# Performance work log

Measured on AMD Instinct MI355X. Metric: run time of the kernel, lower is better.

Reference implementation:

```python
import jax, jax.numpy as jnp
import numpy as np

N = 131072      # total nodes across batched molecular graphs
E = 524288      # directed edges (avg degree ~4)
G = 4096        # number of graphs in the batch
C_IN = 78       # atom feature dim
C_OUT = 128


def _init_linear(key, fan_in, fan_out):
    kw, kb = jax.random.split(key)
    s = 1.0 / np.sqrt(fan_in)
    W = jax.random.uniform(kw, (fan_in, fan_out), jnp.float32, -s, s)
    b = jax.random.uniform(kb, (fan_out,), jnp.float32, -s, s)
    return W, b


def setup_inputs() -> dict:
    key = jax.random.key(0)
    ks = jax.random.split(key, 8)
    x = jax.random.normal(ks[0], (N, C_IN), jnp.float32)
    edge_index = jax.random.randint(ks[1], (2, E), 0, N, dtype=jnp.int32)
    # sorted graph assignment, every graph non-empty (32 nodes per graph)
    batch = ((jnp.arange(N, dtype=jnp.int32) * G) // N).astype(jnp.int32)
    W1, b1 = _init_linear(ks[2], C_IN, C_IN)
    W2, b2 = _init_linear(ks[3], C_IN, 2 * C_IN)
    W3, b3 = _init_linear(ks[4], 2 * C_IN, 4 * C_IN)
    fcW, fcb = _init_linear(ks[5], 4 * C_IN, C_OUT)
    return {"x": x, "edge_index": edge_index, "batch": batch,
            "W1": W1, "b1": b1, "W2": W2, "b2": b2,
            "W3": W3, "b3": b3, "fcW": fcW, "fcb": fcb}


def _gcn_norm(edge_index, n):
    # PyG gcn_norm: add self-loops (weight 1), symmetric D^-1/2 A D^-1/2
    loop = jnp.arange(n, dtype=edge_index.dtype)
    src = jnp.concatenate([edge_index[0], loop])
    dst = jnp.concatenate([edge_index[1], loop])
    deg = jax.ops.segment_sum(jnp.ones_like(dst, jnp.float32), dst, num_segments=n)
    dis = jnp.where(deg > 0, jax.lax.rsqrt(jnp.maximum(deg, 1.0)), 0.0)
    norm = dis[src] * dis[dst]  # [E + N]
    return src, dst, norm


def _gcn_conv(h, W, b, src, dst, norm, n):
    h = h @ W                       # linear transform first (PyG order)
    msg = h[src] * norm[:, None]    # gather + edge-normalize
    agg = jax.ops.segment_sum(msg, dst, num_segments=n)  # scatter-add
    return agg + b


def reference(x, edge_index, batch, W1, b1, W2, b2, W3, b3, fcW, fcb):
    n = x.shape[0]
    src, dst, norm = _gcn_norm(edge_index, n)
    h = jax.nn.relu(_gcn_conv(x, W1, b1, src, dst, norm, n))
    h = jax.nn.relu(_gcn_conv(h, W2, b2, src, dst, norm, n))
    h = jax.nn.relu(_gcn_conv(h, W3, b3, src, dst, norm, n))
    pooled = jax.ops.segment_max(h, batch, num_segments=G)  # global max pool
    out = pooled @ fcW + fcb
    # dropout is identity in eval mode
    return out
```

## Files before the change

### kernel.cpp

```cpp
#include <hip/hip_runtime.h>

#define NN 131072
#define NE 524288
#define NG 4096

typedef __attribute__((ext_vector_type(8))) short bfx8;
typedef __attribute__((ext_vector_type(4))) float f32x4;

static __device__ __forceinline__ ushort f2bf(float f) {
    union { float f; unsigned u; } v; v.f = f;
    unsigned r = (v.u + 0x7fff + ((v.u >> 16) & 1)) >> 16;
    return (ushort)r;
}
static __device__ __forceinline__ float bf2f(short s) {
    union { unsigned u; float f; } v;
    v.u = ((unsigned)(ushort)s) << 16;
    return v.f;
}


__global__ void k_count(const int* __restrict__ dst, int* __restrict__ counts) {
    int e = blockIdx.x * blockDim.x + threadIdx.x;
    if (e < NE) atomicAdd(&counts[dst[e]], 1);
}

__global__ void k_scanA(const int* __restrict__ in, int* __restrict__ out,
                        int* __restrict__ bsum, float* __restrict__ dis) {
    __shared__ int s[256];
    int t = threadIdx.x;
    int i = blockIdx.x * 256 + t;
    int v = in[i];
    dis[i] = rsqrtf((float)(v + 1));
    s[t] = v;
    __syncthreads();
    for (int off = 1; off < 256; off <<= 1) {
        int x = (t >= off) ? s[t - off] : 0;
        __syncthreads();
        s[t] += x;
        __syncthreads();
    }
    out[i] = s[t] - v;
    if (t == 255) bsum[blockIdx.x] = s[t];
}

__global__ void k_scanB(int* __restrict__ bsum) {
    __shared__ int s[512];
    int t = threadIdx.x;
    int v = bsum[t];
    s[t] = v;
    __syncthreads();
    for (int off = 1; off < 512; off <<= 1) {
        int x = (t >= off) ? s[t - off] : 0;
        __syncthreads();
        s[t] += x;
        __syncthreads();
    }
    bsum[t] = s[t] - v;
}

__global__ void k_scanC(int* __restrict__ rowstart, const int* __restrict__ bsum) {
    int t = threadIdx.x;
    int i = blockIdx.x * 256 + t;
    rowstart[i] += bsum[blockIdx.x];
    if (i == 0) rowstart[NN] = NE;
}

__global__ void k_fill(const int* __restrict__ src, const int* __restrict__ dst,
                       const int* __restrict__ rowstart, int* __restrict__ cursor,
                       const float* __restrict__ dis,
                       int* __restrict__ col, float* __restrict__ wgt) {
    int e = blockIdx.x * blockDim.x + threadIdx.x;
    if (e >= NE) return;
    int s = src[e], d = dst[e];
    int pos = rowstart[d] + atomicAdd(&cursor[d], 1);
    col[pos] = s;
    wgt[pos] = dis[s] * dis[d];
}

__global__ void k_prep(const float* __restrict__ x, ushort* __restrict__ xb,
                       const float* __restrict__ W1, ushort* __restrict__ W1T,
                       const float* __restrict__ W2, ushort* __restrict__ W2T,
                       const float* __restrict__ W3, ushort* __restrict__ W3T) {
    int idx = blockIdx.x * 256 + threadIdx.x;
    const int NX = NN * 96;
    if (idx < NX) {
        int i = idx / 96, c = idx - i * 96;
        xb[idx] = (c < 78) ? f2bf(x[i * 78 + c]) : (ushort)0;
        return;
    }
    idx -= NX;
    if (idx < 78 * 96) {
        int n = idx / 96, k = idx - n * 96;
        W1T[idx] = (k < 78) ? f2bf(W1[k * 78 + n]) : (ushort)0;
        return;
    }
    idx -= 78 * 96;
    if (idx < 156 * 96) {
        int n = idx / 96, k = idx - n * 96;
        W2T[idx] = (k < 78) ? f2bf(W2[k * 156 + n]) : (ushort)0;
        return;
    }
    idx -= 156 * 96;
    if (idx < 312 * 160) {
        int n = idx / 160, k = idx - n * 160;
        W3T[idx] = (k < 156) ? f2bf(W3[k * 312 + n]) : (ushort)0;
    }
}


template<int KP, int LCH, int CO, int CPO, bool POOL>
__global__ __launch_bounds__(256)
void k_fused(const ushort* __restrict__ hin, const int* __restrict__ rowstart,
             const int* __restrict__ col, const float* __restrict__ wgt,
             const float* __restrict__ dis,
             const ushort* __restrict__ BT, const float* __restrict__ bias,
             const int* __restrict__ batch,
             ushort* __restrict__ hout, float* __restrict__ pooled) {
    constexpr int NCH = KP / 8;
    constexpr int LP  = LCH * 8;
    constexpr int NP  = (CO + 63) / 64;
    __shared__ ushort sA[64 * LP];

    const int tid  = threadIdx.x;
    const int row0 = blockIdx.x * 64;

    for (int id = tid; id < 64 * NCH; id += 256) {
        int r  = id / NCH, kc = id - r * NCH;
        int i  = row0 + r;
        int ch = kc * 8;
        const ushort* gb = hin + ch;

        float d = dis[i];
        bfx8 self = *(const bfx8*)(hin + (size_t)i * KP + ch);
        float acc[8];
        #pragma unroll
        for (int k = 0; k < 8; ++k) acc[k] = d * d * bf2f(self[k]);

        int j = rowstart[i], j1 = rowstart[i + 1];
        for (; j + 4 <= j1; j += 4) {
            int c0 = col[j], c1 = col[j + 1], c2 = col[j + 2], c3 = col[j + 3];
            float w0 = wgt[j], w1 = wgt[j + 1], w2 = wgt[j + 2], w3 = wgt[j + 3];
            bfx8 g0 = *(const bfx8*)(gb + (size_t)c0 * KP);
            bfx8 g1 = *(const bfx8*)(gb + (size_t)c1 * KP);
            bfx8 g2 = *(const bfx8*)(gb + (size_t)c2 * KP);
            bfx8 g3 = *(const bfx8*)(gb + (size_t)c3 * KP);
            #pragma unroll
            for (int k = 0; k < 8; ++k) {
                acc[k] = fmaf(w0, bf2f(g0[k]), acc[k]);
                acc[k] = fmaf(w1, bf2f(g1[k]), acc[k]);
                acc[k] = fmaf(w2, bf2f(g2[k]), acc[k]);
                acc[k] = fmaf(w3, bf2f(g3[k]), acc[k]);
            }
        }
        for (; j < j1; ++j) {
            int c = col[j];
            float w = wgt[j];
            bfx8 g = *(const bfx8*)(gb + (size_t)c * KP);
            #pragma unroll
            for (int k = 0; k < 8; ++k) acc[k] = fmaf(w, bf2f(g[k]), acc[k]);
        }

        bfx8 ov;
        #pragma unroll
        for (int k = 0; k < 8; ++k) ov[k] = (short)f2bf(acc[k]);
        int swz = (kc & ~7) | ((kc & 7) ^ (r & 7));
        *(bfx8*)(sA + r * LP + swz * 8) = ov;
    }
    __syncthreads();

    const int lane = tid & 63;
    const int wave = tid >> 6;
    const int wr = wave >> 1, wc = wave & 1;
    const int l15 = lane & 15, l4 = lane >> 4;
    const int r7 = l15 & 7;
    const int rowA0 = wr * 32 + l15;
    const int gbase = row0 + wr * 32;
    const int koff = l4 * 8;

    #pragma unroll
    for (int p = 0; p < NP; ++p) {
        const int bc0 = p * 64 + wc * 32 + l15;
        f32x4 acc[2][2] = {};
        #pragma unroll
        for (int ks = 0; ks < KP / 32; ++ks) {
            int chunk = l4 + ks * 4;
            int swz = (chunk & ~7) | ((chunk & 7) ^ r7);
            int off = swz * 8;
            bfx8 a0 = *(const bfx8*)(sA + rowA0 * LP + off);
            bfx8 a1 = *(const bfx8*)(sA + (rowA0 + 16) * LP + off);
            bfx8 b0 = {0,0,0,0,0,0,0,0}, b1 = {0,0,0,0,0,0,0,0};
            if (bc0 < CO)      b0 = *(const bfx8*)(BT + (size_t)bc0 * KP + koff + ks * 32);
            if (bc0 + 16 < CO) b1 = *(const bfx8*)(BT + (size_t)(bc0 + 16) * KP + koff + ks * 32);
            acc[0][0] = __builtin_amdgcn_mfma_f32_16x16x32_bf16(a0, b0, acc[0][0], 0, 0, 0);
            acc[0][1] = __builtin_amdgcn_mfma_f32_16x16x32_bf16(a0, b1, acc[0][1], 0, 0, 0);
            acc[1][0] = __builtin_amdgcn_mfma_f32_16x16x32_bf16(a1, b0, acc[1][0], 0, 0, 0);
            acc[1][1] = __builtin_amdgcn_mfma_f32_16x16x32_bf16(a1, b1, acc[1][1], 0, 0, 0);
        }

        if constexpr (POOL) {
            const bool uni = (batch[gbase] == batch[gbase + 31]);
            #pragma unroll
            for (int fn = 0; fn < 2; ++fn) {
                int cg = p * 64 + wc * 32 + fn * 16 + l15;
                bool cok = cg < CO;
                float bs = cok ? bias[cg] : 0.0f;
                if (uni) {
                    float m = -1e30f;
                    #pragma unroll
                    for (int fm = 0; fm < 2; ++fm)
                        #pragma unroll
                        for (int j = 0; j < 4; ++j)
                            m = fmaxf(m, acc[fm][fn][j]);
                    m = fmaxf(m, __shfl_xor(m, 16));
                    m = fmaxf(m, __shfl_xor(m, 32));
                    if (l4 == 0 && cok) {
                        int g = batch[gbase];
                        float v = fmaxf(m + bs, 0.0f);
                        atomicMax((int*)&pooled[g * CO + cg], __float_as_int(v));
                    }
                } else {
                    #pragma unroll
                    for (int fm = 0; fm < 2; ++fm)
                        #pragma unroll
                        for (int j = 0; j < 4; ++j) {
                            if (cok) {
                                int rg = gbase + fm * 16 + l4 * 4 + j;
                                int g = batch[rg];
                                float v = fmaxf(acc[fm][fn][j] + bs, 0.0f);
                                atomicMax((int*)&pooled[g * CO + cg], __float_as_int(v));
                            }
                        }
                }
            }
        } else {
            #pragma unroll
            for (int fn = 0; fn < 2; ++fn) {
                int cg = p * 64 + wc * 32 + fn * 16 + l15;
                if (cg >= CPO) continue;
                float bs = (cg < CO) ? bias[cg] : 0.0f;
                #pragma unroll
                for (int fm = 0; fm < 2; ++fm)
                    #pragma unroll
                    for (int j = 0; j < 4; ++j) {
                        int row = gbase + fm * 16 + l4 * 4 + j;
                        float v = (cg < CO) ? fmaxf(acc[fm][fn][j] + bs, 0.0f) : 0.0f;
                        hout[(size_t)row * CPO + cg] = f2bf(v);
                    }
            }
        }
    }
}


__global__ __launch_bounds__(256)
void k_fc(const float* __restrict__ pooled, const float* __restrict__ fcW,
          const float* __restrict__ fcb, float* __restrict__ out) {
    __shared__ float sp[8][312];
    const int tid = threadIdx.x;
    const int g0 = blockIdx.x * 8;

    for (int k = tid; k < 8 * 312; k += 256)
        ((float*)sp)[k] = pooled[(size_t)g0 * 312 + k];
    __syncthreads();

    const int half = tid >> 7;
    const int c = tid & 127;
    float b = fcb[c];
    float acc0 = b, acc1 = b, acc2 = b, acc3 = b;
    const float* wp = fcW + c;
    const float* p0 = sp[half * 4 + 0];
    const float* p1 = sp[half * 4 + 1];
    const float* p2 = sp[half * 4 + 2];
    const float* p3 = sp[half * 4 + 3];
    #pragma unroll 4
    for (int k = 0; k < 312; ++k) {
        float w = wp[(size_t)k * 128];
        acc0 = fmaf(p0[k], w, acc0);
        acc1 = fmaf(p1[k], w, acc1);
        acc2 = fmaf(p2[k], w, acc2);
        acc3 = fmaf(p3[k], w, acc3);
    }
    float* o = out + (size_t)(g0 + half * 4) * 128 + c;
    o[0] = acc0; o[128] = acc1; o[256] = acc2; o[384] = acc3;
}


extern "C" void kernel_launch(void* const* d_in, const int* in_sizes, int n_in,
                              void* d_out, int out_size, void* d_ws, size_t ws_size,
                              hipStream_t stream) {
    const float* x    = (const float*)d_in[0];
    const int*   ei   = (const int*)d_in[1];
    const int*   srcv = ei;
    const int*   dstv = ei + NE;
    const int*   batch = (const int*)d_in[2];
    const float* W1 = (const float*)d_in[3];
    const float* b1 = (const float*)d_in[4];
    const float* W2 = (const float*)d_in[5];
    const float* b2 = (const float*)d_in[6];
    const float* W3 = (const float*)d_in[7];
    const float* b3 = (const float*)d_in[8];
    const float* fcW = (const float*)d_in[9];
    const float* fcb = (const float*)d_in[10];
    float* out = (float*)d_out;

    char* ws = (char*)d_ws;
    size_t off = 0;
    auto take = [&](size_t bytes) -> void* {
        void* p = ws + off;
        off += (bytes + 255) & ~(size_t)255;
        return p;
    };
    int*    counts   = (int*)take((size_t)NN * 4);
    int*    cursor   = (int*)take((size_t)NN * 4);
    float*  pooled   = (float*)take((size_t)NG * 312 * 4);
    int*    rowstart = (int*)take((size_t)(NN + 1) * 4);
    float*  dis      = (float*)take((size_t)NN * 4);
    int*    bsum     = (int*)take(512 * 4);
    int*    col      = (int*)take((size_t)NE * 4);
    float*  wgt      = (float*)take((size_t)NE * 4);
    ushort* xb       = (ushort*)take((size_t)NN * 96 * 2);
    ushort* h1       = (ushort*)take((size_t)NN * 96 * 2);
    ushort* h2       = (ushort*)take((size_t)NN * 160 * 2);
    ushort* W1T      = (ushort*)take((size_t)78 * 96 * 2);
    ushort* W2T      = (ushort*)take((size_t)156 * 96 * 2);
    ushort* W3T      = (ushort*)take((size_t)312 * 160 * 2);

    hipMemsetAsync(counts, 0, (size_t)NN * 4 + (size_t)NN * 4 + (size_t)NG * 312 * 4, stream);

    const int PREP_TOTAL = NN * 96 + 78 * 96 + 156 * 96 + 312 * 160;
    k_prep<<<(PREP_TOTAL + 255) / 256, 256, 0, stream>>>(x, xb, W1, W1T, W2, W2T, W3, W3T);

    k_count<<<NE / 256, 256, 0, stream>>>(dstv, counts);
    k_scanA<<<NN / 256, 256, 0, stream>>>(counts, rowstart, bsum, dis);
    k_scanB<<<1, 512, 0, stream>>>(bsum);
    k_scanC<<<NN / 256, 256, 0, stream>>>(rowstart, bsum);
    k_fill<<<NE / 256, 256, 0, stream>>>(srcv, dstv, rowstart, cursor, dis, col, wgt);

    k_fused<96, 16, 78, 96, false><<<NN / 64, 256, 0, stream>>>(
        xb, rowstart, col, wgt, dis, W1T, b1, nullptr, h1, nullptr);
    k_fused<96, 16, 156, 160, false><<<NN / 64, 256, 0, stream>>>(
        h1, rowstart, col, wgt, dis, W2T, b2, nullptr, h2, nullptr);
    k_fused<160, 24, 312, 312, true><<<NN / 64, 256, 0, stream>>>(
        h2, rowstart, col, wgt, dis, W3T, b3, batch, nullptr, pooled);

    k_fc<<<NG / 8, 256, 0, stream>>>(pooled, fcW, fcb, out);
}
```

Baseline: 339.1 us.

## Merge CSR build and prep into one cooperative kernel; widen fused blocks

Merges the weight/feature conversion, degree count, three-stage scan and CSR fill into a single cooperative kernel that uses grid-wide syncs instead of six separate launches. The fused GCN kernels move to 512-thread blocks with 8 waves, each wave covering 16 output columns instead of 32, so the gather phase gets more threads per 64-row tile. The aim is to cut launch overhead and raise parallelism in the gather. The cost is grid.sync barriers, which need all 1024 blocks co-resident, and less B-fragment reuse per wave in the MFMA stage.

```diff
diff --git a/kernel.cpp b/kernel.cpp
--- a/kernel.cpp
+++ b/kernel.cpp
@@ -1,4 +1,7 @@
 #include <hip/hip_runtime.h>
+#include <hip/hip_cooperative_groups.h>
+
+namespace cg = cooperative_groups;
 
 #define NN 131072
 #define NE 524288
@@ -19,97 +22,101 @@
 }
 
 
-__global__ void k_count(const int* __restrict__ dst, int* __restrict__ counts) {
-    int e = blockIdx.x * blockDim.x + threadIdx.x;
-    if (e < NE) atomicAdd(&counts[dst[e]], 1);
-}
-
-__global__ void k_scanA(const int* __restrict__ in, int* __restrict__ out,
-                        int* __restrict__ bsum, float* __restrict__ dis) {
+#define PREP_TOTAL (NN * 96 + 78 * 96 + 156 * 96 + 312 * 160)
+
+__global__ __launch_bounds__(256)
+void k_preproc(const float* __restrict__ x, ushort* __restrict__ xb,
+               const float* __restrict__ W1, ushort* __restrict__ W1T,
+               const float* __restrict__ W2, ushort* __restrict__ W2T,
+               const float* __restrict__ W3, ushort* __restrict__ W3T,
+               const int* __restrict__ src, const int* __restrict__ dst,
+               int* __restrict__ counts, int* __restrict__ rowstart,
+               int* __restrict__ bsum, int* __restrict__ cursor,
+               float* __restrict__ dis, int* __restrict__ col, float* __restrict__ wgt) {
+    cg::grid_group grid = cg::this_grid();
+    const int tid  = threadIdx.x;
+    const int gidx = blockIdx.x * 256 + tid;
+    const int gsz  = gridDim.x * 256;
+
+    for (int e = gidx; e < NE; e += gsz) atomicAdd(&counts[dst[e]], 1);
+    for (int idx = gidx; idx < PREP_TOTAL; idx += gsz) {
+        int t = idx;
+        if (t < NN * 96) {
+            int i = t / 96, c = t - i * 96;
+            xb[t] = (c < 78) ? f2bf(x[i * 78 + c]) : (ushort)0;
+            continue;
+        }
+        t -= NN * 96;
+        if (t < 78 * 96) {
+            int n = t / 96, k = t - n * 96;
+            W1T[t] = (k < 78) ? f2bf(W1[k * 78 + n]) : (ushort)0;
+            continue;
+        }
+        t -= 78 * 96;
+        if (t < 156 * 96) {
+            int n = t / 96, k = t - n * 96;
+            W2T[t] = (k < 78) ? f2bf(W2[k * 156 + n]) : (ushort)0;
+            continue;
+        }
+        t -= 156 * 96;
+        {
+            int n = t / 160, k = t - n * 160;
+            W3T[t] = (k < 156) ? f2bf(W3[k * 312 + n]) : (ushort)0;
+        }
+    }
+    grid.sync();
+
     __shared__ int s[256];
-    int t = threadIdx.x;
-    int i = blockIdx.x * 256 + t;
-    int v = in[i];
-    dis[i] = rsqrtf((float)(v + 1));
-    s[t] = v;
-    __syncthreads();
-    for (int off = 1; off < 256; off <<= 1) {
-        int x = (t >= off) ? s[t - off] : 0;
+    if (blockIdx.x < 512) {
+        int i = blockIdx.x * 256 + tid;
+        int v = counts[i];
+        dis[i] = rsqrtf((float)(v + 1));
+        s[tid] = v;
         __syncthreads();
-        s[t] += x;
+        for (int off = 1; off < 256; off <<= 1) {
+            int xv = (tid >= off) ? s[tid - off] : 0;
+            __syncthreads();
+            s[tid] += xv;
+            __syncthreads();
+        }
+        rowstart[i] = s[tid] - v;
+        if (tid == 255) bsum[blockIdx.x] = s[tid];
+    }
+    grid.sync();
+
+    __shared__ int t2[512];
+    if (blockIdx.x == 0) {
+        int v1 = bsum[tid], v2 = bsum[tid + 256];
+        t2[tid] = v1; t2[tid + 256] = v2;
         __syncthreads();
-    }
-    out[i] = s[t] - v;
-    if (t == 255) bsum[blockIdx.x] = s[t];
-}
-
-__global__ void k_scanB(int* __restrict__ bsum) {
-    __shared__ int s[512];
-    int t = threadIdx.x;
-    int v = bsum[t];
-    s[t] = v;
-    __syncthreads();
-    for (int off = 1; off < 512; off <<= 1) {
-        int x = (t >= off) ? s[t - off] : 0;
-        __syncthreads();
-        s[t] += x;
-        __syncthreads();
-    }
-    bsum[t] = s[t] - v;
-}
-
-__global__ void k_scanC(int* __restrict__ rowstart, const int* __restrict__ bsum) {
-    int t = threadIdx.x;
-    int i = blockIdx.x * 256 + t;
-    rowstart[i] += bsum[blockIdx.x];
-    if (i == 0) rowstart[NN] = NE;
-}
-
-__global__ void k_fill(const int* __restrict__ src, const int* __restrict__ dst,
-                       const int* __restrict__ rowstart, int* __restrict__ cursor,
-                       const float* __restrict__ dis,
-                       int* __restrict__ col, float* __restrict__ wgt) {
-    int e = blockIdx.x * blockDim.x + threadIdx.x;
-    if (e >= NE) return;
-    int s = src[e], d = dst[e];
-    int pos = rowstart[d] + atomicAdd(&cursor[d], 1);
-    col[pos] = s;
-    wgt[pos] = dis[s] * dis[d];
-}
-
-__global__ void k_prep(const float* __restrict__ x, ushort* __restrict__ xb,
-                       const float* __restrict__ W1, ushort* __restrict__ W1T,
-                       const float* __restrict__ W2, ushort* __restrict__ W2T,
-                       const float* __restrict__ W3, ushort* __restrict__ W3T) {
-    int idx = blockIdx.x * 256 + threadIdx.x;
-    const int NX = NN * 96;
-    if (idx < NX) {
-        int i = idx / 96, c = idx - i * 96;
-        xb[idx] = (c < 78) ? f2bf(x[i * 78 + c]) : (ushort)0;
-        return;
-    }
-    idx -= NX;
-    if (idx < 78 * 96) {
-        int n = idx / 96, k = idx - n * 96;
-        W1T[idx] = (k < 78) ? f2bf(W1[k * 78 + n]) : (ushort)0;
-        return;
-    }
-    idx -= 78 * 96;
-    if (idx < 156 * 96) {
-        int n = idx / 96, k = idx - n * 96;
-        W2T[idx] = (k < 78) ? f2bf(W2[k * 156 + n]) : (ushort)0;
-        return;
-    }
-    idx -= 156 * 96;
-    if (idx < 312 * 160) {
-        int n = idx / 160, k = idx - n * 160;
-        W3T[idx] = (k < 156) ? f2bf(W3[k * 312 + n]) : (ushort)0;
+        for (int off = 1; off < 512; off <<= 1) {
+            int a = (tid >= off) ? t2[tid - off] : 0;
+            int b = (tid + 256 >= off) ? t2[tid + 256 - off] : 0;
+            __syncthreads();
+            t2[tid] += a;
+            t2[tid + 256] += b;
+            __syncthreads();
+        }
+        bsum[tid] = t2[tid] - v1;
+        bsum[tid + 256] = t2[tid + 256] - v2;
+    }
+    grid.sync();
+
+    for (int i = gidx; i < NN; i += gsz) rowstart[i] += bsum[i >> 8];
+    if (gidx == 0) rowstart[NN] = NE;
+    grid.sync();
+
+    for (int e = gidx; e < NE; e += gsz) {
+        int sv = src[e], d = dst[e];
+        int pos = rowstart[d] + atomicAdd(&cursor[d], 1);
+        col[pos] = sv;
+        wgt[pos] = dis[sv] * dis[d];
     }
 }
 
 
 template<int KP, int LCH, int CO, int CPO, bool POOL>
-__global__ __launch_bounds__(256)
+__global__ __launch_bounds__(512)
 void k_fused(const ushort* __restrict__ hin, const int* __restrict__ rowstart,
              const int* __restrict__ col, const float* __restrict__ wgt,
              const float* __restrict__ dis,
@@ -124,7 +131,7 @@
     const int tid  = threadIdx.x;
     const int row0 = blockIdx.x * 64;
 
-    for (int id = tid; id < 64 * NCH; id += 256) {
+    for (int id = tid; id < 64 * NCH; id += 512) {
         int r  = id / NCH, kc = id - r * NCH;
         int i  = row0 + r;
         int ch = kc * 8;
@@ -170,7 +177,7 @@
 
     const int lane = tid & 63;
     const int wave = tid >> 6;
-    const int wr = wave >> 1, wc = wave & 1;
+    const int wr = wave >> 2, wc = wave & 3;
     const int l15 = lane & 15, l4 = lane >> 4;
     const int r7 = l15 & 7;
     const int rowA0 = wr * 32 + l15;
@@ -179,8 +186,8 @@
 
     #pragma unroll
     for (int p = 0; p < NP; ++p) {
-        const int bc0 = p * 64 + wc * 32 + l15;
-        f32x4 acc[2][2] = {};
+        const int bc0 = p * 64 + wc * 16 + l15;
+        f32x4 acc[2] = {};
         #pragma unroll
         for (int ks = 0; ks < KP / 32; ++ks) {
             int chunk = l4 + ks * 4;
@@ -188,62 +195,53 @@
             int off = swz * 8;
             bfx8 a0 = *(const bfx8*)(sA + rowA0 * LP + off);
             bfx8 a1 = *(const bfx8*)(sA + (rowA0 + 16) * LP + off);
-            bfx8 b0 = {0,0,0,0,0,0,0,0}, b1 = {0,0,0,0,0,0,0,0};
-            if (bc0 < CO)      b0 = *(const bfx8*)(BT + (size_t)bc0 * KP + koff + ks * 32);
-            if (bc0 + 16 < CO) b1 = *(const bfx8*)(BT + (size_t)(bc0 + 16) * KP + koff + ks * 32);
-            acc[0][0] = __builtin_amdgcn_mfma_f32_16x16x32_bf16(a0, b0, acc[0][0], 0, 0, 0);
-            acc[0][1] = __builtin_amdgcn_mfma_f32_16x16x32_bf16(a0, b1, acc[0][1], 0, 0, 0);
-            acc[1][0] = __builtin_amdgcn_mfma_f32_16x16x32_bf16(a1, b0, acc[1][0], 0, 0, 0);
-            acc[1][1] = __builtin_amdgcn_mfma_f32_16x16x32_bf16(a1, b1, acc[1][1], 0, 0, 0);
-        }
-
+            bfx8 b0 = {0,0,0,0,0,0,0,0};
+            if (bc0 < CO) b0 = *(const bfx8*)(BT + (size_t)bc0 * KP + koff + ks * 32);
+            acc[0] = __builtin_amdgcn_mfma_f32_16x16x32_bf16(a0, b0, acc[0], 0, 0, 0);
+            acc[1] = __builtin_amdgcn_mfma_f32_16x16x32_bf16(a1, b0, acc[1], 0, 0, 0);
+        }
+
+        const int cg = p * 64 + wc * 16 + l15;
         if constexpr (POOL) {
             const bool uni = (batch[gbase] == batch[gbase + 31]);
-            #pragma unroll
-            for (int fn = 0; fn < 2; ++fn) {
-                int cg = p * 64 + wc * 32 + fn * 16 + l15;
-                bool cok = cg < CO;
-                float bs = cok ? bias[cg] : 0.0f;
-                if (uni) {
-                    float m = -1e30f;
+            bool cok = cg < CO;
+            float bs = cok ? bias[cg] : 0.0f;
+            if (uni) {
+                float m = -1e30f;
+                #pragma unroll
+                for (int fm = 0; fm < 2; ++fm)
                     #pragma unroll
-                    for (int fm = 0; fm < 2; ++fm)
-                        #pragma unroll
-                        for (int j = 0; j < 4; ++j)
-                            m = fmaxf(m, acc[fm][fn][j]);
-                    m = fmaxf(m, __shfl_xor(m, 16));
-                    m = fmaxf(m, __shfl_xor(m, 32));
-                    if (l4 == 0 && cok) {
-                        int g = batch[gbase];
-                        float v = fmaxf(m + bs, 0.0f);
-                        atomicMax((int*)&pooled[g * CO + cg], __float_as_int(v));
+                    for (int j = 0; j < 4; ++j)
+                        m = fmaxf(m, acc[fm][j]);
+                m = fmaxf(m, __shfl_xor(m, 16));
+                m = fmaxf(m, __shfl_xor(m, 32));
+                if (l4 == 0 && cok) {
+                    int g = batch[gbase];
+                    float v = fmaxf(m + bs, 0.0f);
+                    atomicMax((int*)&pooled[g * CO + cg], __float_as_int(v));
+                }
+            } else {
+                #pragma unroll
+                for (int fm = 0; fm < 2; ++fm)
+                    #pragma unroll
+                    for (int j = 0; j < 4; ++j) {
+                        if (cok) {
+                            int rg = gbase + fm * 16 + l4 * 4 + j;
+                            int g = batch[rg];
+                            float v = fmaxf(acc[fm][j] + bs, 0.0f);
+                            atomicMax((int*)&pooled[g * CO + cg], __float_as_int(v));
+                        }
                     }
-                } else {
-                    #pragma unroll
-                    for (int fm = 0; fm < 2; ++fm)
-                        #pragma unroll
-                        for (int j = 0; j < 4; ++j) {
-                            if (cok) {
-                                int rg = gbase + fm * 16 + l4 * 4 + j;
-                                int g = batch[rg];
-                                float v = fmaxf(acc[fm][fn][j] + bs, 0.0f);
-                                atomicMax((int*)&pooled[g * CO + cg], __float_as_int(v));
-                            }
-                        }
-                }
             }
         } else {
-            #pragma unroll
-            for (int fn = 0; fn < 2; ++fn) {
-                int cg = p * 64 + wc * 32 + fn * 16 + l15;
-                if (cg >= CPO) continue;
+            if (cg < CPO) {
                 float bs = (cg < CO) ? bias[cg] : 0.0f;
                 #pragma unroll
                 for (int fm = 0; fm < 2; ++fm)
                     #pragma unroll
                     for (int j = 0; j < 4; ++j) {
                         int row = gbase + fm * 16 + l4 * 4 + j;
-                        float v = (cg < CO) ? fmaxf(acc[fm][fn][j] + bs, 0.0f) : 0.0f;
+                        float v = (cg < CO) ? fmaxf(acc[fm][j] + bs, 0.0f) : 0.0f;
                         hout[(size_t)row * CPO + cg] = f2bf(v);
                     }
             }
@@ -327,20 +325,23 @@
 
     hipMemsetAsync(counts, 0, (size_t)NN * 4 + (size_t)NN * 4 + (size_t)NG * 312 * 4, stream);
 
-    const int PREP_TOTAL = NN * 96 + 78 * 96 + 156 * 96 + 312 * 160;
-    k_prep<<<(PREP_TOTAL + 255) / 256, 256, 0, stream>>>(x, xb, W1, W1T, W2, W2T, W3, W3T);
-
-    k_count<<<NE / 256, 256, 0, stream>>>(dstv, counts);
-    k_scanA<<<NN / 256, 256, 0, stream>>>(counts, rowstart, bsum, dis);
-    k_scanB<<<1, 512, 0, stream>>>(bsum);
-    k_scanC<<<NN / 256, 256, 0, stream>>>(rowstart, bsum);
-    k_fill<<<NE / 256, 256, 0, stream>>>(srcv, dstv, rowstart, cursor, dis, col, wgt);
-
-    k_fused<96, 16, 78, 96, false><<<NN / 64, 256, 0, stream>>>(
+    {
+        void* args[] = {
+            (void*)&x, (void*)&xb,
+            (void*)&W1, (void*)&W1T, (void*)&W2, (void*)&W2T, (void*)&W3, (void*)&W3T,
+            (void*)&srcv, (void*)&dstv,
+            (void*)&counts, (void*)&rowstart, (void*)&bsum, (void*)&cursor,
+            (void*)&dis, (void*)&col, (void*)&wgt
+        };
+        hipLaunchCooperativeKernel((const void*)k_preproc, dim3(1024), dim3(256),
+                                   args, 0, stream);
+    }
+
+    k_fused<96, 16, 78, 96, false><<<NN / 64, 512, 0, stream>>>(
         xb, rowstart, col, wgt, dis, W1T, b1, nullptr, h1, nullptr);
-    k_fused<96, 16, 156, 160, false><<<NN / 64, 256, 0, stream>>>(
+    k_fused<96, 16, 156, 160, false><<<NN / 64, 512, 0, stream>>>(
         h1, rowstart, col, wgt, dis, W2T, b2, nullptr, h2, nullptr);
-    k_fused<160, 24, 312, 312, true><<<NN / 64, 256, 0, stream>>>(
+    k_fused<160, 24, 312, 312, true><<<NN / 64, 512, 0, stream>>>(
         h2, rowstart, col, wgt, dis, W3T, b3, batch, nullptr, pooled);
 
     k_fc<<<NG / 8, 256, 0, stream>>>(pooled, fcW, fcb, out);
```

After: 778.8 us. 130% more time.
